# Kernel optimization log

Measured on AMD Instinct MI355X. Metric: run time of the kernel, lower is better.

The kernel has to match this reference:

```python
import jax, jax.numpy as jnp
import numpy as np

B, S, SK = 4, 1024, 1024
Q_IN, KV_IN = 1024, 1024
G, DQ, DV = 16, 64, 64
OUT = Q_IN
EPS = 1e-5


def setup_inputs() -> dict:
    key = jax.random.key(0)
    ks = jax.random.split(key, 12)
    s_q = 1.0 / np.sqrt(Q_IN)
    s_kv = 1.0 / np.sqrt(KV_IN)
    s_p = 1.0 / np.sqrt(G * DV)
    return {
        "Q": jax.random.normal(ks[0], (B, S, Q_IN), jnp.float32),
        "KV": jax.random.normal(ks[1], (B, SK, KV_IN), jnp.float32),
        "Wq": jax.random.normal(ks[2], (G * DQ, Q_IN), jnp.float32) * s_q,
        "bq": jax.random.normal(ks[3], (G * DQ,), jnp.float32) * s_q,
        "Wk": jax.random.normal(ks[4], (G * DQ, KV_IN), jnp.float32) * s_kv,
        "bk": jax.random.normal(ks[5], (G * DQ,), jnp.float32) * s_kv,
        "Wv": jax.random.normal(ks[6], (G * DV, KV_IN), jnp.float32) * s_kv,
        "bv": jax.random.normal(ks[7], (G * DV,), jnp.float32) * s_kv,
        "Wp": jax.random.normal(ks[8], (OUT, G * DV), jnp.float32) * s_p,
        "bp": jax.random.normal(ks[9], (OUT,), jnp.float32) * s_p,
        "gamma": jnp.ones((OUT,), jnp.float32),
        "beta": jnp.zeros((OUT,), jnp.float32),
    }


def reference(Q, KV, Wq, bq, Wk, bk, Wv, bv, Wp, bp, gamma, beta):
    b, s, _ = Q.shape
    sk = KV.shape[1]
    inv_sqrt_dim = DQ ** (-0.5)

    # projections
    q = Q @ Wq.T + bq            # [b, s, G*DQ]
    k = KV @ Wk.T + bk           # [b, sk, G*DQ]
    v = KV @ Wv.T + bv           # [b, sk, G*DV]

    # q/k: group is the SLOW axis; v: group is the FAST axis (faithful to source)
    q = q.reshape(b, s, G, DQ)               # [b, s, g, d]
    k = k.reshape(b, sk, G, DQ)              # [b, sk, g, d]
    v = v.reshape(b, sk, DV, G)              # [b, sk, d, g]

    logits = jnp.einsum('bsgd,btgd->bgst', q, k) * inv_sqrt_dim  # [b, g, s, sk]
    scores = jax.nn.softmax(logits, axis=-1)
    attn = jnp.einsum('bgst,btdg->bgsd', scores, v)              # [b, g, s, dv]

    # flatten as (dv, g): feature index = d*G + g  (faithful to source permute)
    attn = attn.transpose(0, 2, 3, 1).reshape(b, s, DV * G)
    out = attn @ Wp.T + bp + Q

    # LayerNorm
    mu = out.mean(axis=-1, keepdims=True)
    var = out.var(axis=-1, keepdims=True)
    out = (out - mu) * jax.lax.rsqrt(var + EPS) * gamma + beta

    return out, scores.reshape(b * G, s, sk)
```

## Files before the change

kernel.cpp:

```cpp
#include <hip/hip_runtime.h>

typedef __attribute__((ext_vector_type(8))) short short8;
typedef __attribute__((ext_vector_type(4))) short s16x4;
typedef __attribute__((ext_vector_type(4))) float f32x4;

static __device__ __forceinline__ short f2bf(float x) {
  union { float f; unsigned u; } v; v.f = x;
  unsigned r = (v.u + 0x7fffu + ((v.u >> 16) & 1u)) >> 16;
  return (short)r;
}
static __device__ __forceinline__ float bf2f(short x) {
  union { unsigned u; float f; } v; v.u = ((unsigned)(unsigned short)x) << 16;
  return v.f;
}

static __device__ __forceinline__ void gld16(const short* g, short* l) {
  __builtin_amdgcn_global_load_lds(
      (const __attribute__((address_space(1))) unsigned*)g,
      (__attribute__((address_space(3))) unsigned*)l, 16, 0, 0);
}

__global__ __launch_bounds__(256) void convert_f32_bf16(const float* __restrict__ src,
                                                        short* __restrict__ dst, int n8,
                                                        float scale) {
  int i = blockIdx.x * 256 + threadIdx.x;
  if (i >= n8) return;
  const f32x4* s = (const f32x4*)(src + (long)i * 8);
  f32x4 a = s[0], b = s[1];
  short8 o;
  o[0] = f2bf(a[0] * scale); o[1] = f2bf(a[1] * scale);
  o[2] = f2bf(a[2] * scale); o[3] = f2bf(a[3] * scale);
  o[4] = f2bf(b[0] * scale); o[5] = f2bf(b[1] * scale);
  o[6] = f2bf(b[2] * scale); o[7] = f2bf(b[3] * scale);
  *(short8*)(dst + (long)i * 8) = o;
}

__global__ __launch_bounds__(256) void scale_bias(const float* __restrict__ src,
                                                  float* __restrict__ dst) {
  int i = blockIdx.x * 256 + threadIdx.x;
  dst[i] = src[i] * 0.125f;
}

__global__ __launch_bounds__(256) void convert_permute_wp(const float* __restrict__ src,
                                                          short* __restrict__ dst) {
  __shared__ float row[1024];
  const long o = blockIdx.x;
  *(f32x4*)&row[threadIdx.x * 4] = *(const f32x4*)(src + o * 1024 + threadIdx.x * 4);
  __syncthreads();
  const int f0 = threadIdx.x * 4;
  s16x4 t;
#pragma unroll
  for (int j = 0; j < 4; ++j) {
    int f = f0 + j;
    t[j] = f2bf(row[((f & 63) << 4) + (f >> 6)]);
  }
  *(s16x4*)(dst + o * 1024 + f0) = t;
}

template <int OMODE, typename OutT>
__global__ __launch_bounds__(256, 4) void gemm_mfma(
    const short* __restrict__ A, int lda,
    const short* __restrict__ B, int ldb,
    OutT* __restrict__ Cb, int ldc,
    const float* __restrict__ bias,
    const float* __restrict__ resid, int ldres,
    float scale, int K, int nbn) {
  __shared__ short As[2][64 * 64];
  __shared__ short Bs[2][64 * 64];

  const int nwg = gridDim.x, cpx = nwg >> 3;
  int bid = blockIdx.x;
  bid = (bid & 7) * cpx + (bid >> 3);
  const int bn = (bid % nbn) * 64, bm = (bid / nbn) * 64;

  const int tid = threadIdx.x, lane = tid & 63, wave = tid >> 6;
  const int fr = lane & 15, khi = lane >> 4;

  f32x4 acc[4];
#pragma unroll
  for (int n = 0; n < 4; ++n) acc[n] = (f32x4){0.f, 0.f, 0.f, 0.f};

  auto stage = [&](int buf, int k0) {
#pragma unroll
    for (int it = 0; it < 2; ++it) {
      int l = it * 256 + tid;
      int r = l >> 3, c = (l & 7) ^ (r & 7);
      gld16(A + (long)(bm + r) * lda + k0 + c * 8, &As[buf][l * 8]);
      gld16(B + (long)(bn + r) * ldb + k0 + c * 8, &Bs[buf][l * 8]);
    }
  };

  stage(0, 0);
  __syncthreads();
  int cur = 0;
  for (int k0 = 0; k0 < K; k0 += 64) {
    if (k0 + 64 < K) stage(cur ^ 1, k0 + 64);
#pragma unroll
    for (int ks = 0; ks < 64; ks += 32) {
      const int cc = (ks >> 3) + khi;
      const int ar = wave * 16 + fr;
      short8 af = *(const short8*)&As[cur][ar * 64 + (cc ^ (ar & 7)) * 8];
#pragma unroll
      for (int n = 0; n < 4; ++n) {
        const int br = n * 16 + fr;
        short8 bf = *(const short8*)&Bs[cur][br * 64 + (cc ^ (br & 7)) * 8];
        acc[n] = __builtin_amdgcn_mfma_f32_16x16x32_bf16(af, bf, acc[n], 0, 0, 0);
      }
    }
    __syncthreads();
    cur ^= 1;
  }

  const int col0 = lane & 15, row0 = (lane >> 4) * 4;
#pragma unroll
  for (int n = 0; n < 4; ++n) {
    int gcol = bn + n * 16 + col0;
    float bi = bias ? bias[gcol] : 0.f;
#pragma unroll
    for (int i = 0; i < 4; ++i) {
      int grow = bm + wave * 16 + row0 + i;
      float v = acc[n][i] * scale + bi;
      if (resid) v += resid[(long)grow * ldres + gcol];
      long addr;
      if (OMODE == 0)
        addr = (long)grow * ldc + gcol;
      else
        addr = ((long)(grow >> 10) << 20) + ((long)gcol << 10) + (grow & 1023);
      if constexpr (sizeof(OutT) == 2)
        Cb[addr] = (OutT)f2bf(v);
      else
        Cb[addr] = v;
    }
  }
}

__global__ __launch_bounds__(512, 6) void fused_attn(
    const short* __restrict__ qb,
    const short* __restrict__ kb,
    const short* __restrict__ vt,
    float* __restrict__ scores,
    short* __restrict__ at) {
  constexpr int LP = 72;
  __shared__ short Ks[2][64 * 64];
  __shared__ short Vs[2][64 * 64];
  __shared__ short Ps[128 * LP];

  int bid = blockIdx.x;
  bid = (bid & 7) * 64 + (bid >> 3);
  const int z = bid >> 3, b = z >> 4, g = z & 15;
  const int q0 = (bid & 7) * 128;

  const int tid = threadIdx.x, lane = tid & 63, w = tid >> 6;
  const int fr = lane & 15, khi = lane >> 4;
  const long bqk = (long)b << 20;
  const int qr = q0 + w * 16;

  const short* qrow = qb + bqk + (long)(qr + fr) * 1024 + g * 64 + khi * 8;
  const short8 aq0 = *(const short8*)qrow;
  const short8 aq1 = *(const short8*)(qrow + 32);
  const short* kgp = kb + bqk + g * 64;
  const short* vgp = vt + bqk;

  const int srr = tid >> 3, ssc = ((tid & 7) ^ (srr & 7)) * 8;

  float s4[4] = {0.f, 0.f, 0.f, 0.f};
  gld16(kgp + (long)srr * 1024 + ssc, &Ks[0][tid * 8]);
  __syncthreads();
  int cur = 0;
  for (int t0 = 0; t0 < 1024; t0 += 64) {
    if (t0 < 960)
      gld16(kgp + (long)(t0 + 64 + srr) * 1024 + ssc, &Ks[cur ^ 1][tid * 8]);
    f32x4 sacc[4];
#pragma unroll
    for (int nf = 0; nf < 4; ++nf) sacc[nf] = (f32x4){0.f, 0.f, 0.f, 0.f};
#pragma unroll
    for (int nf = 0; nf < 4; ++nf) {
      const int r2 = nf * 16 + fr;
      short8 b0 = *(const short8*)&Ks[cur][r2 * 64 + (khi ^ (r2 & 7)) * 8];
      short8 b1 = *(const short8*)&Ks[cur][r2 * 64 + ((khi + 4) ^ (r2 & 7)) * 8];
      sacc[nf] = __builtin_amdgcn_mfma_f32_16x16x32_bf16(aq0, b0, sacc[nf], 0, 0, 0);
      sacc[nf] = __builtin_amdgcn_mfma_f32_16x16x32_bf16(aq1, b1, sacc[nf], 0, 0, 0);
    }
#pragma unroll
    for (int nf = 0; nf < 4; ++nf)
#pragma unroll
      for (int i = 0; i < 4; ++i) s4[i] += __expf(sacc[nf][i]);
    __syncthreads();
    cur ^= 1;
  }
#pragma unroll
  for (int i = 0; i < 4; ++i) {
    s4[i] += __shfl_xor(s4[i], 1);
    s4[i] += __shfl_xor(s4[i], 2);
    s4[i] += __shfl_xor(s4[i], 4);
    s4[i] += __shfl_xor(s4[i], 8);
  }
  float inv4[4];
#pragma unroll
  for (int i = 0; i < 4; ++i) inv4[i] = 1.f / s4[i];

  f32x4 pacc[4];
#pragma unroll
  for (int nv = 0; nv < 4; ++nv) pacc[nv] = (f32x4){0.f, 0.f, 0.f, 0.f};

  gld16(kgp + (long)srr * 1024 + ssc, &Ks[0][tid * 8]);
  gld16(vgp + ((long)(srr * 16 + g) << 10) + ssc, &Vs[0][tid * 8]);
  __syncthreads();
  cur = 0;
  for (int t0 = 0; t0 < 1024; t0 += 64) {
    if (t0 < 960) {
      gld16(kgp + (long)(t0 + 64 + srr) * 1024 + ssc, &Ks[cur ^ 1][tid * 8]);
      gld16(vgp + ((long)(srr * 16 + g) << 10) + t0 + 64 + ssc, &Vs[cur ^ 1][tid * 8]);
    }
    f32x4 sacc[4];
#pragma unroll
    for (int nf = 0; nf < 4; ++nf) sacc[nf] = (f32x4){0.f, 0.f, 0.f, 0.f};
#pragma unroll
    for (int nf = 0; nf < 4; ++nf) {
      const int r2 = nf * 16 + fr;
      short8 b0 = *(const short8*)&Ks[cur][r2 * 64 + (khi ^ (r2 & 7)) * 8];
      short8 b1 = *(const short8*)&Ks[cur][r2 * 64 + ((khi + 4) ^ (r2 & 7)) * 8];
      sacc[nf] = __builtin_amdgcn_mfma_f32_16x16x32_bf16(aq0, b0, sacc[nf], 0, 0, 0);
      sacc[nf] = __builtin_amdgcn_mfma_f32_16x16x32_bf16(aq1, b1, sacc[nf], 0, 0, 0);
    }
#pragma unroll
    for (int nf = 0; nf < 4; ++nf)
#pragma unroll
      for (int i = 0; i < 4; ++i)
        Ps[(w * 16 + khi * 4 + i) * LP + nf * 16 + fr] =
            f2bf(__expf(sacc[nf][i]) * inv4[i]);

#pragma unroll
    for (int ks = 0; ks < 64; ks += 32) {
      const int cc = (ks >> 3) + khi;
      short8 ap = *(const short8*)&Ps[(w * 16 + fr) * LP + ks + khi * 8];
#pragma unroll
      for (int nv = 0; nv < 4; ++nv) {
        const int dr = nv * 16 + fr;
        short8 bvv = *(const short8*)&Vs[cur][dr * 64 + (cc ^ (dr & 7)) * 8];
        pacc[nv] = __builtin_amdgcn_mfma_f32_16x16x32_bf16(ap, bvv, pacc[nv], 0, 0, 0);
      }
    }

#pragma unroll
    for (int ri = 0; ri < 4; ++ri) {
      const int row = ri * 4 + khi;
      s16x4 pv4 = *(const s16x4*)&Ps[(w * 16 + row) * LP + fr * 4];
      f32x4 o;
      o[0] = bf2f(pv4[0]); o[1] = bf2f(pv4[1]);
      o[2] = bf2f(pv4[2]); o[3] = bf2f(pv4[3]);
      *(f32x4*)&scores[((long)z << 20) + ((long)(qr + row) << 10) + t0 + fr * 4] = o;
    }
    __syncthreads();
    cur ^= 1;
  }

#pragma unroll
  for (int nv = 0; nv < 4; ++nv)
#pragma unroll
    for (int i = 0; i < 4; ++i)
      at[bqk + ((long)(qr + khi * 4 + i) << 10) + g * 64 + nv * 16 + fr] =
          f2bf(pacc[nv][i]);
}

__global__ __launch_bounds__(256) void layernorm_rows(const float* __restrict__ X,
                                                      const float* __restrict__ gamma,
                                                      const float* __restrict__ beta,
                                                      float* __restrict__ O) {
  const int row = blockIdx.x * 4 + (threadIdx.x >> 6);
  const int lane = threadIdx.x & 63;
  const float* x = X + (long)row * 1024 + lane * 4;
  f32x4 v[4];
  float s = 0.f, sq = 0.f;
#pragma unroll
  for (int j = 0; j < 4; ++j) {
    v[j] = *(const f32x4*)(x + j * 256);
#pragma unroll
    for (int e = 0; e < 4; ++e) {
      s += v[j][e];
      sq += v[j][e] * v[j][e];
    }
  }
#pragma unroll
  for (int off = 32; off; off >>= 1) {
    s += __shfl_xor(s, off);
    sq += __shfl_xor(sq, off);
  }
  const float mu = s * (1.f / 1024.f);
  const float var = sq * (1.f / 1024.f) - mu * mu;
  const float rstd = rsqrtf(var + 1e-5f);
  float* o = O + (long)row * 1024 + lane * 4;
#pragma unroll
  for (int j = 0; j < 4; ++j) {
    f32x4 g = *(const f32x4*)(gamma + lane * 4 + j * 256);
    f32x4 be = *(const f32x4*)(beta + lane * 4 + j * 256);
    f32x4 r;
#pragma unroll
    for (int e = 0; e < 4; ++e) r[e] = (v[j][e] - mu) * rstd * g[e] + be[e];
    *(f32x4*)(o + j * 256) = r;
  }
}

extern "C" void kernel_launch(void* const* d_in, const int* in_sizes, int n_in,
                              void* d_out, int out_size, void* d_ws, size_t ws_size,
                              hipStream_t stream) {
  const float* Q = (const float*)d_in[0];
  const float* KV = (const float*)d_in[1];
  const float* Wq = (const float*)d_in[2];
  const float* bq = (const float*)d_in[3];
  const float* Wk = (const float*)d_in[4];
  const float* bk = (const float*)d_in[5];
  const float* Wv = (const float*)d_in[6];
  const float* bv = (const float*)d_in[7];
  const float* Wp = (const float*)d_in[8];
  const float* bp = (const float*)d_in[9];
  const float* gamma = (const float*)d_in[10];
  const float* beta = (const float*)d_in[11];

  float* out = (float*)d_out;
  float* scores = out + (long)4 * 1024 * 1024;

  char* ws = (char*)d_ws;
  short* Wqb = (short*)(ws);
  short* Wkb = (short*)(ws + (2L << 20));
  short* Wvb = (short*)(ws + (4L << 20));
  short* Wpb = (short*)(ws + (6L << 20));
  short* qb  = (short*)(ws + (8L << 20));
  short* kb  = (short*)(ws + (16L << 20));
  short* vt  = (short*)(ws + (24L << 20));
  short* at  = (short*)(ws + (32L << 20));
  float* pre = (float*)(ws + (40L << 20));
  short* Qb  = (short*)(ws + (40L << 20));
  short* KVb = (short*)(ws + (48L << 20));
  float* bqs = (float*)(ws + (56L << 20));
  (void)ws_size; (void)in_sizes; (void)n_in; (void)out_size;

  convert_f32_bf16<<<2048, 256, 0, stream>>>(Q, Qb, 524288, 1.f);
  convert_f32_bf16<<<2048, 256, 0, stream>>>(KV, KVb, 524288, 1.f);
  convert_f32_bf16<<<512, 256, 0, stream>>>(Wq, Wqb, 131072, 0.125f);
  convert_f32_bf16<<<512, 256, 0, stream>>>(Wk, Wkb, 131072, 1.f);
  convert_f32_bf16<<<512, 256, 0, stream>>>(Wv, Wvb, 131072, 1.f);
  convert_permute_wp<<<1024, 256, 0, stream>>>(Wp, Wpb);
  scale_bias<<<4, 256, 0, stream>>>(bq, bqs);

  gemm_mfma<0, short><<<1024, 256, 0, stream>>>(
      Qb, 1024, Wqb, 1024, qb, 1024, bqs, nullptr, 0, 1.f, 1024, 16);
  gemm_mfma<0, short><<<1024, 256, 0, stream>>>(
      KVb, 1024, Wkb, 1024, kb, 1024, bk, nullptr, 0, 1.f, 1024, 16);
  gemm_mfma<1, short><<<1024, 256, 0, stream>>>(
      KVb, 1024, Wvb, 1024, vt, 1024, bv, nullptr, 0, 1.f, 1024, 16);

  fused_attn<<<512, 512, 0, stream>>>(qb, kb, vt, scores, at);

  gemm_mfma<0, float><<<1024, 256, 0, stream>>>(
      at, 1024, Wpb, 1024, pre, 1024, bp, Q, 1024, 1.f, 1024, 16);

  layernorm_rows<<<1024, 256, 0, stream>>>(pre, gamma, beta, out);
}
```

Baseline: 193.1 us.

## Merge prep kernels, batch QKV projections, enlarge GEMM tiles to 128x128

Folds the seven conversion and bias-scale launches into a single prep kernel that dispatches on block index. The three projection GEMMs become one launch, and GEMM tiles grow from 64x64 to 128x128, with each wave computing a 4x4 grid of MFMA tiles. The bigger tiles raise operand reuse from LDS, and the merged launches cut launch overhead. In exchange, register and LDS use per block goes up, and the output GEMM now runs only 256 blocks, which may underfill the GPU.

```diff
diff --git a/kernel.cpp b/kernel.cpp
--- a/kernel.cpp
+++ b/kernel.cpp
@@ -20,11 +20,9 @@
       (__attribute__((address_space(3))) unsigned*)l, 16, 0, 0);
 }
 
-__global__ __launch_bounds__(256) void convert_f32_bf16(const float* __restrict__ src,
-                                                        short* __restrict__ dst, int n8,
-                                                        float scale) {
-  int i = blockIdx.x * 256 + threadIdx.x;
-  if (i >= n8) return;
+static __device__ __forceinline__ void conv8(const float* __restrict__ src,
+                                             short* __restrict__ dst, int i,
+                                             float scale) {
   const f32x4* s = (const f32x4*)(src + (long)i * 8);
   f32x4 a = s[0], b = s[1];
   short8 o;
@@ -35,77 +33,96 @@
   *(short8*)(dst + (long)i * 8) = o;
 }
 
-__global__ __launch_bounds__(256) void scale_bias(const float* __restrict__ src,
-                                                  float* __restrict__ dst) {
-  int i = blockIdx.x * 256 + threadIdx.x;
-  dst[i] = src[i] * 0.125f;
-}
-
-__global__ __launch_bounds__(256) void convert_permute_wp(const float* __restrict__ src,
-                                                          short* __restrict__ dst) {
-  __shared__ float row[1024];
-  const long o = blockIdx.x;
-  *(f32x4*)&row[threadIdx.x * 4] = *(const f32x4*)(src + o * 1024 + threadIdx.x * 4);
-  __syncthreads();
-  const int f0 = threadIdx.x * 4;
-  s16x4 t;
-#pragma unroll
-  for (int j = 0; j < 4; ++j) {
-    int f = f0 + j;
-    t[j] = f2bf(row[((f & 63) << 4) + (f >> 6)]);
-  }
-  *(s16x4*)(dst + o * 1024 + f0) = t;
-}
-
-template <int OMODE, typename OutT>
-__global__ __launch_bounds__(256, 4) void gemm_mfma(
-    const short* __restrict__ A, int lda,
-    const short* __restrict__ B, int ldb,
-    OutT* __restrict__ Cb, int ldc,
-    const float* __restrict__ bias,
-    const float* __restrict__ resid, int ldres,
-    float scale, int K, int nbn) {
-  __shared__ short As[2][64 * 64];
-  __shared__ short Bs[2][64 * 64];
-
-  const int nwg = gridDim.x, cpx = nwg >> 3;
-  int bid = blockIdx.x;
-  bid = (bid & 7) * cpx + (bid >> 3);
-  const int bn = (bid % nbn) * 64, bm = (bid / nbn) * 64;
-
+__global__ __launch_bounds__(256) void prep(
+    const float* __restrict__ Q, const float* __restrict__ KV,
+    const float* __restrict__ Wq, const float* __restrict__ Wk,
+    const float* __restrict__ Wv, const float* __restrict__ Wp,
+    const float* __restrict__ bq,
+    short* __restrict__ Qb, short* __restrict__ KVb,
+    short* __restrict__ Wqb, short* __restrict__ Wkb,
+    short* __restrict__ Wvb, short* __restrict__ Wpb,
+    float* __restrict__ bqs) {
+  const int blk = blockIdx.x, tid = threadIdx.x;
+  if (blk < 2048) {
+    conv8(Q, Qb, blk * 256 + tid, 1.f);
+  } else if (blk < 4096) {
+    conv8(KV, KVb, (blk - 2048) * 256 + tid, 1.f);
+  } else if (blk < 4608) {
+    conv8(Wq, Wqb, (blk - 4096) * 256 + tid, 0.125f);
+  } else if (blk < 5120) {
+    conv8(Wk, Wkb, (blk - 4608) * 256 + tid, 1.f);
+  } else if (blk < 5632) {
+    conv8(Wv, Wvb, (blk - 5120) * 256 + tid, 1.f);
+  } else if (blk < 6656) {
+    __shared__ float row[1024];
+    const long o = blk - 5632;
+    *(f32x4*)&row[tid * 4] = *(const f32x4*)(Wp + o * 1024 + tid * 4);
+    __syncthreads();
+    const int f0 = tid * 4;
+    s16x4 t;
+#pragma unroll
+    for (int j = 0; j < 4; ++j) {
+      int f = f0 + j;
+      t[j] = f2bf(row[((f & 63) << 4) + (f >> 6)]);
+    }
+    *(s16x4*)(Wpb + o * 1024 + f0) = t;
+  } else {
+    int i = (blk - 6656) * 256 + tid;
+    bqs[i] = bq[i] * 0.125f;
+  }
+}
+
+template <typename OutT>
+static __device__ __forceinline__ void gemm_core(
+    const short* __restrict__ A, const short* __restrict__ B,
+    OutT* __restrict__ C, const float* __restrict__ bias,
+    const float* __restrict__ resid, int bm, int bn, int omode,
+    short (*As)[128 * 64], short (*Bs)[128 * 64]) {
   const int tid = threadIdx.x, lane = tid & 63, wave = tid >> 6;
   const int fr = lane & 15, khi = lane >> 4;
-
-  f32x4 acc[4];
-#pragma unroll
-  for (int n = 0; n < 4; ++n) acc[n] = (f32x4){0.f, 0.f, 0.f, 0.f};
+  const int wr = wave >> 1, wc = wave & 1;
+
+  f32x4 acc[4][4];
+#pragma unroll
+  for (int m = 0; m < 4; ++m)
+#pragma unroll
+    for (int n = 0; n < 4; ++n) acc[m][n] = (f32x4){0.f, 0.f, 0.f, 0.f};
 
   auto stage = [&](int buf, int k0) {
 #pragma unroll
-    for (int it = 0; it < 2; ++it) {
+    for (int it = 0; it < 4; ++it) {
       int l = it * 256 + tid;
       int r = l >> 3, c = (l & 7) ^ (r & 7);
-      gld16(A + (long)(bm + r) * lda + k0 + c * 8, &As[buf][l * 8]);
-      gld16(B + (long)(bn + r) * ldb + k0 + c * 8, &Bs[buf][l * 8]);
+      gld16(A + (long)(bm + r) * 1024 + k0 + c * 8, &As[buf][l * 8]);
+      gld16(B + (long)(bn + r) * 1024 + k0 + c * 8, &Bs[buf][l * 8]);
     }
   };
 
   stage(0, 0);
   __syncthreads();
   int cur = 0;
-  for (int k0 = 0; k0 < K; k0 += 64) {
-    if (k0 + 64 < K) stage(cur ^ 1, k0 + 64);
+  for (int k0 = 0; k0 < 1024; k0 += 64) {
+    if (k0 < 960) stage(cur ^ 1, k0 + 64);
 #pragma unroll
     for (int ks = 0; ks < 64; ks += 32) {
       const int cc = (ks >> 3) + khi;
-      const int ar = wave * 16 + fr;
-      short8 af = *(const short8*)&As[cur][ar * 64 + (cc ^ (ar & 7)) * 8];
+      short8 af[4], bf[4];
+#pragma unroll
+      for (int m = 0; m < 4; ++m) {
+        const int ar = wr * 64 + m * 16 + fr;
+        af[m] = *(const short8*)&As[cur][ar * 64 + ((cc ^ (ar & 7)) * 8)];
+      }
 #pragma unroll
       for (int n = 0; n < 4; ++n) {
-        const int br = n * 16 + fr;
-        short8 bf = *(const short8*)&Bs[cur][br * 64 + (cc ^ (br & 7)) * 8];
-        acc[n] = __builtin_amdgcn_mfma_f32_16x16x32_bf16(af, bf, acc[n], 0, 0, 0);
+        const int br = wc * 64 + n * 16 + fr;
+        bf[n] = *(const short8*)&Bs[cur][br * 64 + ((cc ^ (br & 7)) * 8)];
       }
+#pragma unroll
+      for (int m = 0; m < 4; ++m)
+#pragma unroll
+        for (int n = 0; n < 4; ++n)
+          acc[m][n] = __builtin_amdgcn_mfma_f32_16x16x32_bf16(af[m], bf[n],
+                                                              acc[m][n], 0, 0, 0);
     }
     __syncthreads();
     cur ^= 1;
@@ -113,25 +130,61 @@
 
   const int col0 = lane & 15, row0 = (lane >> 4) * 4;
 #pragma unroll
-  for (int n = 0; n < 4; ++n) {
-    int gcol = bn + n * 16 + col0;
-    float bi = bias ? bias[gcol] : 0.f;
-#pragma unroll
-    for (int i = 0; i < 4; ++i) {
-      int grow = bm + wave * 16 + row0 + i;
-      float v = acc[n][i] * scale + bi;
-      if (resid) v += resid[(long)grow * ldres + gcol];
-      long addr;
-      if (OMODE == 0)
-        addr = (long)grow * ldc + gcol;
-      else
-        addr = ((long)(grow >> 10) << 20) + ((long)gcol << 10) + (grow & 1023);
-      if constexpr (sizeof(OutT) == 2)
-        Cb[addr] = (OutT)f2bf(v);
-      else
-        Cb[addr] = v;
-    }
-  }
+  for (int m = 0; m < 4; ++m) {
+#pragma unroll
+    for (int n = 0; n < 4; ++n) {
+      const int gcol = bn + wc * 64 + n * 16 + col0;
+      const float bi = bias[gcol];
+#pragma unroll
+      for (int i = 0; i < 4; ++i) {
+        const int grow = bm + wr * 64 + m * 16 + row0 + i;
+        float v = acc[m][n][i] + bi;
+        if (resid) v += resid[(long)grow * 1024 + gcol];
+        long addr;
+        if (omode == 0)
+          addr = (long)grow * 1024 + gcol;
+        else
+          addr = ((long)(grow >> 10) << 20) + ((long)gcol << 10) + (grow & 1023);
+        if constexpr (sizeof(OutT) == 2)
+          C[addr] = (OutT)f2bf(v);
+        else
+          C[addr] = v;
+      }
+    }
+  }
+}
+
+__global__ __launch_bounds__(256, 2) void proj_all(
+    const short* __restrict__ Qb, const short* __restrict__ KVb,
+    const short* __restrict__ Wqb, const short* __restrict__ Wkb,
+    const short* __restrict__ Wvb,
+    const float* __restrict__ bqs, const float* __restrict__ bk,
+    const float* __restrict__ bv,
+    short* __restrict__ qb, short* __restrict__ kb, short* __restrict__ vt) {
+  __shared__ short As[2][128 * 64];
+  __shared__ short Bs[2][128 * 64];
+  int bid = blockIdx.x;
+  int swz = (bid & 7) * 96 + (bid >> 3);
+  const int seg = swz >> 8, local = swz & 255;
+  const int bm = (local >> 3) * 128, bn = (local & 7) * 128;
+  if (seg == 0)
+    gemm_core<short>(Qb, Wqb, qb, bqs, nullptr, bm, bn, 0, As, Bs);
+  else if (seg == 1)
+    gemm_core<short>(KVb, Wkb, kb, bk, nullptr, bm, bn, 0, As, Bs);
+  else
+    gemm_core<short>(KVb, Wvb, vt, bv, nullptr, bm, bn, 1, As, Bs);
+}
+
+__global__ __launch_bounds__(256, 2) void out_gemm(
+    const short* __restrict__ at, const short* __restrict__ Wpb,
+    const float* __restrict__ bp, const float* __restrict__ Q,
+    float* __restrict__ pre) {
+  __shared__ short As[2][128 * 64];
+  __shared__ short Bs[2][128 * 64];
+  int bid = blockIdx.x;
+  int swz = (bid & 7) * 32 + (bid >> 3);
+  const int bm = (swz >> 3) * 128, bn = (swz & 7) * 128;
+  gemm_core<float>(at, Wpb, pre, bp, Q, bm, bn, 0, As, Bs);
 }
 
 __global__ __launch_bounds__(512, 6) void fused_attn(
@@ -335,25 +388,15 @@
   float* bqs = (float*)(ws + (56L << 20));
   (void)ws_size; (void)in_sizes; (void)n_in; (void)out_size;
 
-  convert_f32_bf16<<<2048, 256, 0, stream>>>(Q, Qb, 524288, 1.f);
-  convert_f32_bf16<<<2048, 256, 0, stream>>>(KV, KVb, 524288, 1.f);
-  convert_f32_bf16<<<512, 256, 0, stream>>>(Wq, Wqb, 131072, 0.125f);
-  convert_f32_bf16<<<512, 256, 0, stream>>>(Wk, Wkb, 131072, 1.f);
-  convert_f32_bf16<<<512, 256, 0, stream>>>(Wv, Wvb, 131072, 1.f);
-  convert_permute_wp<<<1024, 256, 0, stream>>>(Wp, Wpb);
-  scale_bias<<<4, 256, 0, stream>>>(bq, bqs);
-
-  gemm_mfma<0, short><<<1024, 256, 0, stream>>>(
-      Qb, 1024, Wqb, 1024, qb, 1024, bqs, nullptr, 0, 1.f, 1024, 16);
-  gemm_mfma<0, short><<<1024, 256, 0, stream>>>(
-      KVb, 1024, Wkb, 1024, kb, 1024, bk, nullptr, 0, 1.f, 1024, 16);
-  gemm_mfma<1, short><<<1024, 256, 0, stream>>>(
-      KVb, 1024, Wvb, 1024, vt, 1024, bv, nullptr, 0, 1.f, 1024, 16);
+  prep<<<6660, 256, 0, stream>>>(Q, KV, Wq, Wk, Wv, Wp, bq,
+                                 Qb, KVb, Wqb, Wkb, Wvb, Wpb, bqs);
+
+  proj_all<<<768, 256, 0, stream>>>(Qb, KVb, Wqb, Wkb, Wvb, bqs, bk, bv,
+                                    qb, kb, vt);
 
   fused_attn<<<512, 512, 0, stream>>>(qb, kb, vt, scores, at);
 
-  gemm_mfma<0, float><<<1024, 256, 0, stream>>>(
-      at, 1024, Wpb, 1024, pre, 1024, bp, Q, 1024, 1.f, 1024, 16);
+  out_gemm<<<256, 256, 0, stream>>>(at, Wpb, bp, Q, pre);
 
   layernorm_rows<<<1024, 256, 0, stream>>>(pre, gamma, beta, out);
 }
```

Measured after the change: 179.2 us. 1.08x faster.
